# Performance work log

Hardware: AMD Instinct MI355X
Metric: run time of the kernel (lower is better)

The kernel has to match this reference:

```python
import jax, jax.numpy as jnp
import numpy as np

N = 50000
E = 800000
IN_DIM = 256
HID = 128
OUT = 64


def setup_inputs() -> dict:
    key = jax.random.key(0)
    ks = jax.random.split(key, 12)
    inp = {}
    inp["x"] = jax.random.normal(ks[0], (N, IN_DIM), dtype=jnp.float32)
    inp["edge_index"] = jax.random.randint(ks[1], (2, E), 0, N, dtype=jnp.int64)
    s0 = 1.0 / np.sqrt(IN_DIM)
    inp["W0"] = jax.random.uniform(ks[2], (IN_DIM, HID), jnp.float32, -s0, s0)
    inp["b0"] = jax.random.uniform(ks[3], (HID,), jnp.float32, -s0, s0)
    sa = 1.0 / np.sqrt(2 * HID)
    inp["att_w1"] = jax.random.uniform(ks[4], (2 * HID, 1), jnp.float32, -sa, sa)
    inp["att_b1"] = jax.random.uniform(ks[5], (1,), jnp.float32, -sa, sa)
    inp["eps1"] = jnp.float32(0.1)
    inp["att_w2"] = jax.random.uniform(ks[6], (2 * HID, 1), jnp.float32, -sa, sa)
    inp["att_b2"] = jax.random.uniform(ks[7], (1,), jnp.float32, -sa, sa)
    inp["eps2"] = jnp.float32(0.1)
    sc = 1.0 / np.sqrt(HID)
    inp["Wc"] = jax.random.uniform(ks[8], (HID, OUT), jnp.float32, -sc, sc)
    inp["bc"] = jax.random.uniform(ks[9], (OUT,), jnp.float32, -sc, sc)
    return inp


def _fagcn_layer(x, row, col, att_w, att_b, eps):
    # x: [N, H]; row/col: [E]
    x_i = x[row]                       # [E, H] source (gathered)
    x_j = x[col]                       # [E, H] destination
    # cat([x_i, x_j]) @ att_w == x_i @ att_w[:H] + x_j @ att_w[H:]
    H = x.shape[1]
    score = x_i @ att_w[:H] + x_j @ att_w[H:] + att_b  # [E, 1]
    alpha = jnp.tanh(score)            # [E, 1]
    messages = alpha * x_i             # [E, H]
    agg = jax.ops.segment_sum(messages, col, num_segments=x.shape[0])  # [N, H]
    return eps * x + (1.0 - eps) * agg


def reference(x, edge_index, W0, b0, att_w1, att_b1, eps1, att_w2, att_b2, eps2, Wc, bc):
    row, col = edge_index[0], edge_index[1]
    h = jax.nn.relu(x @ W0 + b0)       # initial linear + relu (dropout=eval identity)
    h = jax.nn.relu(_fagcn_layer(h, row, col, att_w1, att_b1, eps1))
    h = jax.nn.relu(_fagcn_layer(h, row, col, att_w2, att_b2, eps2))
    return h @ Wc + bc                 # [N, OUT]
```

## Files before the change

### kernel.cpp

```cpp
#include <hip/hip_runtime.h>

#define N_NODES 50000
#define E_EDGES 800000
#define IN_DIM 256
#define HID 128
#define OUT_DIM 64
#define SLOT 64

#define LR 64
#define KS 64
#define KP 72
#define HP 136

#define NBUILD ((E_EDGES / 8 + 255) / 256)
#define NLIN ((N_NODES + LR - 1) / LR)

typedef unsigned short u16;
typedef __attribute__((ext_vector_type(8))) short short8;
typedef __attribute__((ext_vector_type(4))) float floatx4;

__device__ __forceinline__ u16 f2bf(float f) {
    unsigned u = __float_as_uint(f);
    unsigned r = (u + 0x7FFFu + ((u >> 16) & 1u)) >> 16;
    return (u16)r;
}
__device__ __forceinline__ void bf8_unpack(uint4 v, float* f) {
    f[0] = __uint_as_float(v.x << 16); f[1] = __uint_as_float(v.x & 0xffff0000u);
    f[2] = __uint_as_float(v.y << 16); f[3] = __uint_as_float(v.y & 0xffff0000u);
    f[4] = __uint_as_float(v.z << 16); f[5] = __uint_as_float(v.z & 0xffff0000u);
    f[6] = __uint_as_float(v.w << 16); f[7] = __uint_as_float(v.w & 0xffff0000u);
}
__device__ __forceinline__ uint4 bf8_pack(const float* f) {
    uint4 o;
    o.x = f2bf(f[0]) | ((unsigned)f2bf(f[1]) << 16);
    o.y = f2bf(f[2]) | ((unsigned)f2bf(f[3]) << 16);
    o.z = f2bf(f[4]) | ((unsigned)f2bf(f[5]) << 16);
    o.w = f2bf(f[6]) | ((unsigned)f2bf(f[7]) << 16);
    return o;
}

__global__ __launch_bounds__(256) void k_front(
    const float* __restrict__ x, const float* __restrict__ W0,
    const float* __restrict__ b0, const float* __restrict__ aw1,
    u16* __restrict__ h, float* __restrict__ sa, float* __restrict__ sb,
    const int* __restrict__ ei, int* __restrict__ cnt,
    u16* __restrict__ srcidx, const float* __restrict__ Wc,
    u16* __restrict__ Wct) {
    __shared__ u16 As[LR][KP];
    __shared__ u16 Bs[HID][KP];

    if (blockIdx.x < NBUILD) {
        const int gid = blockIdx.x * 256 + threadIdx.x;
        if (gid < HID * OUT_DIM)
            Wct[gid] = f2bf(Wc[(gid & 127) * OUT_DIM + (gid >> 7)]);
        if (gid >= E_EDGES / 8) return;
        const int4 w0 = ((const int4*)ei)[2 * gid];
        const int4 w1 = ((const int4*)ei)[2 * gid + 1];
        const int4 c0 = ((const int4*)(ei + E_EDGES))[2 * gid];
        const int4 c1 = ((const int4*)(ei + E_EDGES))[2 * gid + 1];
        const int p0 = atomicAdd(&cnt[c0.x], 1);
        const int p1 = atomicAdd(&cnt[c0.y], 1);
        const int p2 = atomicAdd(&cnt[c0.z], 1);
        const int p3 = atomicAdd(&cnt[c0.w], 1);
        const int p4 = atomicAdd(&cnt[c1.x], 1);
        const int p5 = atomicAdd(&cnt[c1.y], 1);
        const int p6 = atomicAdd(&cnt[c1.z], 1);
        const int p7 = atomicAdd(&cnt[c1.w], 1);
        if (p0 < SLOT) srcidx[(c0.x << 6) + p0] = (u16)w0.x;
        if (p1 < SLOT) srcidx[(c0.y << 6) + p1] = (u16)w0.y;
        if (p2 < SLOT) srcidx[(c0.z << 6) + p2] = (u16)w0.z;
        if (p3 < SLOT) srcidx[(c0.w << 6) + p3] = (u16)w0.w;
        if (p4 < SLOT) srcidx[(c1.x << 6) + p4] = (u16)w1.x;
        if (p5 < SLOT) srcidx[(c1.y << 6) + p5] = (u16)w1.y;
        if (p6 < SLOT) srcidx[(c1.z << 6) + p6] = (u16)w1.z;
        if (p7 < SLOT) srcidx[(c1.w << 6) + p7] = (u16)w1.w;
        return;
    }

    const int t = threadIdx.x;
    const int lane = t & 63;
    const int w = t >> 6;
    const int sub = lane & 15;
    const int quad = lane >> 4;
    const int row0 = (blockIdx.x - NBUILD) * LR;

    floatx4 acc[8];
    #pragma unroll
    for (int i = 0; i < 8; ++i) acc[i] = (floatx4){0.f, 0.f, 0.f, 0.f};

    const int ar = t >> 2;
    const int ak = (t & 3) * 16;
    const int sr = t >> 1;
    const int sk = (t & 1) * 32;

    for (int k0 = 0; k0 < IN_DIM; k0 += KS) {
        {
            int gr = row0 + ar;
            if (gr > N_NODES - 1) gr = N_NODES - 1;
            const float* src = x + (size_t)gr * IN_DIM + k0 + ak;
            #pragma unroll
            for (int i = 0; i < 2; ++i) {
                float4 f0 = ((const float4*)src)[2 * i];
                float4 f1 = ((const float4*)src)[2 * i + 1];
                uint4 p;
                p.x = f2bf(f0.x) | ((unsigned)f2bf(f0.y) << 16);
                p.y = f2bf(f0.z) | ((unsigned)f2bf(f0.w) << 16);
                p.z = f2bf(f1.x) | ((unsigned)f2bf(f1.y) << 16);
                p.w = f2bf(f1.z) | ((unsigned)f2bf(f1.w) << 16);
                *(uint4*)&As[ar][ak + 8 * i] = p;
            }
            const float* wp = W0 + (size_t)(k0 + sk) * HID + sr;
            #pragma unroll
            for (int i = 0; i < 4; ++i) {
                uint4 p;
                unsigned q[4];
                #pragma unroll
                for (int j = 0; j < 4; ++j) {
                    const float lo = wp[(i * 8 + 2 * j) * HID];
                    const float hi = wp[(i * 8 + 2 * j + 1) * HID];
                    q[j] = f2bf(lo) | ((unsigned)f2bf(hi) << 16);
                }
                p.x = q[0]; p.y = q[1]; p.z = q[2]; p.w = q[3];
                *(uint4*)&Bs[sr][sk + 8 * i] = p;
            }
        }
        __syncthreads();
        #pragma unroll
        for (int kk = 0; kk < KS; kk += 32) {
            short8 a0 = *(const short8*)&As[w * 16 + sub][kk + quad * 8];
            #pragma unroll
            for (int ct = 0; ct < 8; ++ct) {
                short8 bb = *(const short8*)&Bs[ct * 16 + sub][kk + quad * 8];
                acc[ct] = __builtin_amdgcn_mfma_f32_16x16x32_bf16(a0, bb, acc[ct], 0, 0, 0);
            }
        }
        __syncthreads();
    }

    float bias[8], w1c[8], w2c[8];
    #pragma unroll
    for (int ct = 0; ct < 8; ++ct) {
        const int col = ct * 16 + sub;
        bias[ct] = b0[col];
        w1c[ct] = aw1[col];
        w2c[ct] = aw1[HID + col];
    }
    #pragma unroll
    for (int reg = 0; reg < 4; ++reg) {
        const int gr = row0 + w * 16 + quad * 4 + reg;
        const bool ok = gr < N_NODES;
        float ps = 0.f, pd = 0.f;
        #pragma unroll
        for (int ct = 0; ct < 8; ++ct) {
            const float val = fmaxf(acc[ct][reg] + bias[ct], 0.f);
            if (ok) h[(size_t)gr * HID + ct * 16 + sub] = f2bf(val);
            ps += val * w1c[ct];
            pd += val * w2c[ct];
        }
        #pragma unroll
        for (int off = 1; off < 16; off <<= 1) {
            ps += __shfl_xor(ps, off);
            pd += __shfl_xor(pd, off);
        }
        if (sub == 0 && ok) { sa[gr] = ps; sb[gr] = pd; }
    }
}

__global__ __launch_bounds__(256) void k_agg(const u16* __restrict__ hin,
                                             const float* __restrict__ sa,
                                             const float* __restrict__ sb,
                                             const float* __restrict__ attb,
                                             const float* __restrict__ epsp,
                                             const int* __restrict__ cnt,
                                             const u16* __restrict__ srcidx,
                                             u16* __restrict__ hout,
                                             const float* __restrict__ attw_next,
                                             float* __restrict__ sa_next,
                                             float* __restrict__ sb_next) {
    const int qid = threadIdx.x >> 4;
    const int sub = threadIdx.x & 15;
    const int n = blockIdx.x * 16 + qid;
    if (n >= N_NODES) return;
    const float b = attb[0];
    const float sbn = sb[n];
    const int beg = n << 6;
    int deg = cnt[n];
    if (deg > SLOT) deg = SLOT;
    const int end = beg + deg;
    float acc[8];
    #pragma unroll
    for (int j = 0; j < 8; ++j) acc[j] = 0.f;

    int e = beg;
    uint4 svn;
    if (e + 8 <= end) svn = *(const uint4*)(srcidx + e);
    for (; e + 8 <= end; e += 8) {
        const uint4 sv = svn;
        if (e + 16 <= end) svn = *(const uint4*)(srcidx + e + 8);
        int s[8];
        s[0] = (int)(sv.x & 0xffffu); s[1] = (int)(sv.x >> 16);
        s[2] = (int)(sv.y & 0xffffu); s[3] = (int)(sv.y >> 16);
        s[4] = (int)(sv.z & 0xffffu); s[5] = (int)(sv.z >> 16);
        s[6] = (int)(sv.w & 0xffffu); s[7] = (int)(sv.w >> 16);
        uint4 v[8];
        #pragma unroll
        for (int i = 0; i < 8; ++i)
            v[i] = *(const uint4*)(hin + (size_t)s[i] * HID + sub * 8);
        const float tt = tanhf(sa[s[sub & 7]] + sbn + b);
        float al[8];
        #pragma unroll
        for (int i = 0; i < 8; ++i) al[i] = __shfl(tt, i, 16);
        #pragma unroll
        for (int i = 0; i < 8; ++i) {
            float f[8];
            bf8_unpack(v[i], f);
            #pragma unroll
            for (int j = 0; j < 8; ++j) acc[j] += al[i] * f[j];
        }
    }
    const int rem = end - e;
    if (rem > 0) {
        const int sfirst = (int)srcidx[e];
        int s[8];
        #pragma unroll
        for (int i = 0; i < 8; ++i) s[i] = (i < rem) ? (int)srcidx[e + i] : sfirst;
        const float tt = ((sub & 7) < rem) ? tanhf(sa[s[sub & 7]] + sbn + b) : 0.f;
        float al[8];
        #pragma unroll
        for (int i = 0; i < 8; ++i) al[i] = __shfl(tt, i, 16);
        #pragma unroll
        for (int i = 0; i < 8; ++i) {
            if (i < rem) {
                const uint4 v = *(const uint4*)(hin + (size_t)s[i] * HID + sub * 8);
                float f[8];
                bf8_unpack(v, f);
                #pragma unroll
                for (int j = 0; j < 8; ++j) acc[j] += al[i] * f[j];
            }
        }
    }

    const float eps = epsp[0];
    const float om = 1.f - eps;
    const uint4 sv = *(const uint4*)(hin + (size_t)n * HID + sub * 8);
    float self[8], hv[8];
    bf8_unpack(sv, self);
    #pragma unroll
    for (int j = 0; j < 8; ++j)
        hv[j] = fmaxf(eps * self[j] + om * acc[j], 0.f);
    *(uint4*)(hout + (size_t)n * HID + sub * 8) = bf8_pack(hv);

    if (attw_next != nullptr) {
        float psum = 0.f, dsum = 0.f;
        #pragma unroll
        for (int j = 0; j < 8; ++j) {
            psum += hv[j] * attw_next[sub * 8 + j];
            dsum += hv[j] * attw_next[HID + sub * 8 + j];
        }
        #pragma unroll
        for (int off = 1; off < 16; off <<= 1) {
            psum += __shfl_xor(psum, off);
            dsum += __shfl_xor(dsum, off);
        }
        if (sub == 0) { sa_next[n] = psum; sb_next[n] = dsum; }
    }
}

__global__ __launch_bounds__(256) void k_out_mfma(const u16* __restrict__ h,
                                                  const u16* __restrict__ Wct,
                                                  const float* __restrict__ bc,
                                                  float* __restrict__ out) {
    __shared__ u16 Hs[LR][HP];
    const int t = threadIdx.x;
    const int lane = t & 63;
    const int w = t >> 6;
    const int sub = lane & 15;
    const int quad = lane >> 4;
    const int row0 = blockIdx.x * LR;

    {
        const int hr = t >> 2;
        const int hc = (t & 3) * 32;
        int gr = row0 + hr;
        if (gr > N_NODES - 1) gr = N_NODES - 1;
        const u16* src = h + (size_t)gr * HID + hc;
        #pragma unroll
        for (int i = 0; i < 4; ++i)
            *(uint4*)&Hs[hr][hc + 8 * i] = ((const uint4*)src)[i];
    }
    __syncthreads();

    floatx4 acc[4];
    #pragma unroll
    for (int j = 0; j < 4; ++j) acc[j] = (floatx4){0.f, 0.f, 0.f, 0.f};

    #pragma unroll
    for (int ks = 0; ks < 4; ++ks) {
        const int ko = ks * 32 + quad * 8;
        short8 a = *(const short8*)&Hs[w * 16 + sub][ko];
        #pragma unroll
        for (int ct = 0; ct < 4; ++ct) {
            short8 bb = *(const short8*)(Wct + (ct * 16 + sub) * HID + ko);
            acc[ct] = __builtin_amdgcn_mfma_f32_16x16x32_bf16(a, bb, acc[ct], 0, 0, 0);
        }
    }

    #pragma unroll
    for (int ct = 0; ct < 4; ++ct) {
        const float bias = bc[ct * 16 + sub];
        #pragma unroll
        for (int reg = 0; reg < 4; ++reg) {
            const int gr = row0 + w * 16 + quad * 4 + reg;
            if (gr < N_NODES)
                out[(size_t)gr * OUT_DIM + ct * 16 + sub] = acc[ct][reg] + bias;
        }
    }
}

extern "C" void kernel_launch(void* const* d_in, const int* in_sizes, int n_in,
                              void* d_out, int out_size, void* d_ws, size_t ws_size,
                              hipStream_t stream) {
    const float* x   = (const float*)d_in[0];
    const int*   ei  = (const int*)d_in[1];
    const float* W0  = (const float*)d_in[2];
    const float* b0  = (const float*)d_in[3];
    const float* aw1 = (const float*)d_in[4];
    const float* ab1 = (const float*)d_in[5];
    const float* e1  = (const float*)d_in[6];
    const float* aw2 = (const float*)d_in[7];
    const float* ab2 = (const float*)d_in[8];
    const float* e2  = (const float*)d_in[9];
    const float* Wc  = (const float*)d_in[10];
    const float* bc  = (const float*)d_in[11];
    float* out = (float*)d_out;

    u16* hA  = (u16*)d_ws;
    u16* hB  = hA + (size_t)N_NODES * HID;
    u16* Wct = hB + (size_t)N_NODES * HID;
    float* sa1 = (float*)(Wct + HID * OUT_DIM);
    float* sb1 = sa1 + N_NODES;
    float* sa2 = sb1 + N_NODES;
    float* sb2 = sa2 + N_NODES;
    int* cnt    = (int*)(sb2 + N_NODES);
    u16* srcidx = (u16*)(cnt + N_NODES);

    hipMemsetAsync(cnt, 0, N_NODES * sizeof(int), stream);
    k_front<<<NBUILD + NLIN, 256, 0, stream>>>(x, W0, b0, aw1, hA, sa1, sb1,
                                               ei, cnt, srcidx, Wc, Wct);
    k_agg<<<(N_NODES + 15) / 16, 256, 0, stream>>>(hA, sa1, sb1, ab1, e1, cnt, srcidx,
                                                   hB, aw2, sa2, sb2);
    k_agg<<<(N_NODES + 15) / 16, 256, 0, stream>>>(hB, sa2, sb2, ab2, e2, cnt, srcidx,
                                                   hA, nullptr, nullptr, nullptr);
    k_out_mfma<<<(N_NODES + LR - 1) / LR, 256, 0, stream>>>(hA, Wct, bc, out);
}
```

Baseline: 243.5 us.

## Fuse output linear layer into second aggregation kernel

Removes the separate MFMA output kernel and computes h@Wc+bc directly inside the second aggregation pass, using Wc staged in shared memory per block and lane shuffles to broadcast hidden values. This avoids writing and re-reading the final hidden tensor and one kernel launch, and drops the Wc transpose in the front kernel. In exchange every block reloads the full fp32 Wc into LDS (34KB), which may reduce occupancy of the latency-bound gather, and the projection now uses scalar FMAs instead of matrix cores.

```diff
diff --git a/kernel.cpp b/kernel.cpp
--- a/kernel.cpp
+++ b/kernel.cpp
@@ -10,7 +10,7 @@
 #define LR 64
 #define KS 64
 #define KP 72
-#define HP 136
+#define WCP 68
 
 #define NBUILD ((E_EDGES / 8 + 255) / 256)
 #define NLIN ((N_NODES + LR - 1) / LR)
@@ -44,15 +44,12 @@
     const float* __restrict__ b0, const float* __restrict__ aw1,
     u16* __restrict__ h, float* __restrict__ sa, float* __restrict__ sb,
     const int* __restrict__ ei, int* __restrict__ cnt,
-    u16* __restrict__ srcidx, const float* __restrict__ Wc,
-    u16* __restrict__ Wct) {
+    u16* __restrict__ srcidx) {
     __shared__ u16 As[LR][KP];
     __shared__ u16 Bs[HID][KP];
 
     if (blockIdx.x < NBUILD) {
         const int gid = blockIdx.x * 256 + threadIdx.x;
-        if (gid < HID * OUT_DIM)
-            Wct[gid] = f2bf(Wc[(gid & 127) * OUT_DIM + (gid >> 7)]);
         if (gid >= E_EDGES / 8) return;
         const int4 w0 = ((const int4*)ei)[2 * gid];
         const int4 w1 = ((const int4*)ei)[2 * gid + 1];
@@ -166,6 +163,7 @@
     }
 }
 
+template <bool FUSE_OUT>
 __global__ __launch_bounds__(256) void k_agg(const u16* __restrict__ hin,
                                              const float* __restrict__ sa,
                                              const float* __restrict__ sb,
@@ -176,7 +174,19 @@
                                              u16* __restrict__ hout,
                                              const float* __restrict__ attw_next,
                                              float* __restrict__ sa_next,
-                                             float* __restrict__ sb_next) {
+                                             float* __restrict__ sb_next,
+                                             const float* __restrict__ Wc,
+                                             const float* __restrict__ bc,
+                                             float* __restrict__ outp) {
+    __shared__ float Wcs[FUSE_OUT ? HID * WCP : 1];
+    if constexpr (FUSE_OUT) {
+        for (int i = threadIdx.x; i < HID * (OUT_DIM / 4); i += 256) {
+            const int k = i >> 4, c = (i & 15) << 2;
+            *(float4*)&Wcs[k * WCP + c] = *(const float4*)(Wc + k * OUT_DIM + c);
+        }
+        __syncthreads();
+    }
+
     const int qid = threadIdx.x >> 4;
     const int sub = threadIdx.x & 15;
     const int n = blockIdx.x * 16 + qid;
@@ -248,9 +258,9 @@
     #pragma unroll
     for (int j = 0; j < 8; ++j)
         hv[j] = fmaxf(eps * self[j] + om * acc[j], 0.f);
-    *(uint4*)(hout + (size_t)n * HID + sub * 8) = bf8_pack(hv);
-
-    if (attw_next != nullptr) {
+
+    if constexpr (!FUSE_OUT) {
+        *(uint4*)(hout + (size_t)n * HID + sub * 8) = bf8_pack(hv);
         float psum = 0.f, dsum = 0.f;
         #pragma unroll
         for (int j = 0; j < 8; ++j) {
@@ -263,57 +273,19 @@
             dsum += __shfl_xor(dsum, off);
         }
         if (sub == 0) { sa_next[n] = psum; sb_next[n] = dsum; }
-    }
-}
-
-__global__ __launch_bounds__(256) void k_out_mfma(const u16* __restrict__ h,
-                                                  const u16* __restrict__ Wct,
-                                                  const float* __restrict__ bc,
-                                                  float* __restrict__ out) {
-    __shared__ u16 Hs[LR][HP];
-    const int t = threadIdx.x;
-    const int lane = t & 63;
-    const int w = t >> 6;
-    const int sub = lane & 15;
-    const int quad = lane >> 4;
-    const int row0 = blockIdx.x * LR;
-
-    {
-        const int hr = t >> 2;
-        const int hc = (t & 3) * 32;
-        int gr = row0 + hr;
-        if (gr > N_NODES - 1) gr = N_NODES - 1;
-        const u16* src = h + (size_t)gr * HID + hc;
-        #pragma unroll
-        for (int i = 0; i < 4; ++i)
-            *(uint4*)&Hs[hr][hc + 8 * i] = ((const uint4*)src)[i];
-    }
-    __syncthreads();
-
-    floatx4 acc[4];
-    #pragma unroll
-    for (int j = 0; j < 4; ++j) acc[j] = (floatx4){0.f, 0.f, 0.f, 0.f};
-
-    #pragma unroll
-    for (int ks = 0; ks < 4; ++ks) {
-        const int ko = ks * 32 + quad * 8;
-        short8 a = *(const short8*)&Hs[w * 16 + sub][ko];
-        #pragma unroll
-        for (int ct = 0; ct < 4; ++ct) {
-            short8 bb = *(const short8*)(Wct + (ct * 16 + sub) * HID + ko);
-            acc[ct] = __builtin_amdgcn_mfma_f32_16x16x32_bf16(a, bb, acc[ct], 0, 0, 0);
-        }
-    }
-
-    #pragma unroll
-    for (int ct = 0; ct < 4; ++ct) {
-        const float bias = bc[ct * 16 + sub];
-        #pragma unroll
-        for (int reg = 0; reg < 4; ++reg) {
-            const int gr = row0 + w * 16 + quad * 4 + reg;
-            if (gr < N_NODES)
-                out[(size_t)gr * OUT_DIM + ct * 16 + sub] = acc[ct][reg] + bias;
-        }
+    } else {
+        float p0 = 0.f, p1 = 0.f, p2 = 0.f, p3 = 0.f;
+        #pragma unroll
+        for (int k = 0; k < HID; ++k) {
+            const float hvk = __shfl(hv[k & 7], k >> 3, 16);
+            const float4 wc = *(const float4*)&Wcs[k * WCP + sub * 4];
+            p0 += hvk * wc.x; p1 += hvk * wc.y;
+            p2 += hvk * wc.z; p3 += hvk * wc.w;
+        }
+        const float4 bb = *(const float4*)(bc + sub * 4);
+        float4 o4;
+        o4.x = p0 + bb.x; o4.y = p1 + bb.y; o4.z = p2 + bb.z; o4.w = p3 + bb.w;
+        *(float4*)(outp + (size_t)n * OUT_DIM + sub * 4) = o4;
     }
 }
 
@@ -336,8 +308,7 @@
 
     u16* hA  = (u16*)d_ws;
     u16* hB  = hA + (size_t)N_NODES * HID;
-    u16* Wct = hB + (size_t)N_NODES * HID;
-    float* sa1 = (float*)(Wct + HID * OUT_DIM);
+    float* sa1 = (float*)(hB + (size_t)N_NODES * HID);
     float* sb1 = sa1 + N_NODES;
     float* sa2 = sb1 + N_NODES;
     float* sb2 = sa2 + N_NODES;
@@ -346,10 +317,11 @@
 
     hipMemsetAsync(cnt, 0, N_NODES * sizeof(int), stream);
     k_front<<<NBUILD + NLIN, 256, 0, stream>>>(x, W0, b0, aw1, hA, sa1, sb1,
-                                               ei, cnt, srcidx, Wc, Wct);
-    k_agg<<<(N_NODES + 15) / 16, 256, 0, stream>>>(hA, sa1, sb1, ab1, e1, cnt, srcidx,
-                                                   hB, aw2, sa2, sb2);
-    k_agg<<<(N_NODES + 15) / 16, 256, 0, stream>>>(hB, sa2, sb2, ab2, e2, cnt, srcidx,
-                                                   hA, nullptr, nullptr, nullptr);
-    k_out_mfma<<<(N_NODES + LR - 1) / LR, 256, 0, stream>>>(hA, Wct, bc, out);
-}
+                                               ei, cnt, srcidx);
+    k_agg<false><<<(N_NODES + 15) / 16, 256, 0, stream>>>(
+        hA, sa1, sb1, ab1, e1, cnt, srcidx, hB, aw2, sa2, sb2,
+        nullptr, nullptr, nullptr);
+    k_agg<true><<<(N_NODES + 15) / 16, 256, 0, stream>>>(
+        hB, sa2, sb2, ab2, e2, cnt, srcidx, nullptr, nullptr, nullptr, nullptr,
+        Wc, bc, out);
+}
```

New measurement: 249.4 us. 2.4% more time.

## Pre-transpose weights to bf16 and feed MFMA operands directly from global memory

Applied to the files above, without the earlier changes.

Adds a small prep kernel that zeroes the degree counters in place of the memset and converts W0 and Wc into transposed bf16 layouts. The front linear layer and the output layer then drop their shared-memory staging and barriers, loading A fragments straight from x or h and B fragments from the transposed weights held in L2/L1. This removes the per-block strided fp32 W0 reads and conversions, the LDS traffic and the syncthreads, at the cost of one more launch and redundant per-wave global loads of the weight tiles.

```diff
diff --git a/kernel.cpp b/kernel.cpp
--- a/kernel.cpp
+++ b/kernel.cpp
@@ -8,10 +8,6 @@
 #define SLOT 64
 
 #define LR 64
-#define KS 64
-#define KP 72
-#define HP 136
-
 #define NBUILD ((E_EDGES / 8 + 255) / 256)
 #define NLIN ((N_NODES + LR - 1) / LR)
 
@@ -39,20 +35,31 @@
     return o;
 }
 
+__global__ __launch_bounds__(256) void k_pre(const float* __restrict__ W0,
+                                             const float* __restrict__ Wc,
+                                             u16* __restrict__ W0T,
+                                             u16* __restrict__ Wct,
+                                             int* __restrict__ cnt) {
+    const int gid = blockIdx.x * 256 + threadIdx.x;
+    if (gid < N_NODES / 4) ((int4*)cnt)[gid] = (int4){0, 0, 0, 0};
+    if (gid < IN_DIM * HID) {
+        const int n = gid >> 8, k = gid & (IN_DIM - 1);
+        W0T[gid] = f2bf(W0[k * HID + n]);
+    }
+    if (gid < HID * OUT_DIM) {
+        const int o = gid >> 7, k = gid & (HID - 1);
+        Wct[gid] = f2bf(Wc[k * OUT_DIM + o]);
+    }
+}
+
 __global__ __launch_bounds__(256) void k_front(
-    const float* __restrict__ x, const float* __restrict__ W0,
+    const float* __restrict__ x, const u16* __restrict__ W0T,
     const float* __restrict__ b0, const float* __restrict__ aw1,
     u16* __restrict__ h, float* __restrict__ sa, float* __restrict__ sb,
     const int* __restrict__ ei, int* __restrict__ cnt,
-    u16* __restrict__ srcidx, const float* __restrict__ Wc,
-    u16* __restrict__ Wct) {
-    __shared__ u16 As[LR][KP];
-    __shared__ u16 Bs[HID][KP];
-
+    u16* __restrict__ srcidx) {
     if (blockIdx.x < NBUILD) {
         const int gid = blockIdx.x * 256 + threadIdx.x;
-        if (gid < HID * OUT_DIM)
-            Wct[gid] = f2bf(Wc[(gid & 127) * OUT_DIM + (gid >> 7)]);
         if (gid >= E_EDGES / 8) return;
         const int4 w0 = ((const int4*)ei)[2 * gid];
         const int4 w1 = ((const int4*)ei)[2 * gid + 1];
@@ -84,57 +91,29 @@
     const int quad = lane >> 4;
     const int row0 = (blockIdx.x - NBUILD) * LR;
 
+    int gr_a = row0 + w * 16 + sub;
+    if (gr_a > N_NODES - 1) gr_a = N_NODES - 1;
+    const float* xrow = x + (size_t)gr_a * IN_DIM + quad * 8;
+    const u16* wbase = W0T + (size_t)sub * IN_DIM + quad * 8;
+
     floatx4 acc[8];
     #pragma unroll
     for (int i = 0; i < 8; ++i) acc[i] = (floatx4){0.f, 0.f, 0.f, 0.f};
 
-    const int ar = t >> 2;
-    const int ak = (t & 3) * 16;
-    const int sr = t >> 1;
-    const int sk = (t & 1) * 32;
-
-    for (int k0 = 0; k0 < IN_DIM; k0 += KS) {
-        {
-            int gr = row0 + ar;
-            if (gr > N_NODES - 1) gr = N_NODES - 1;
-            const float* src = x + (size_t)gr * IN_DIM + k0 + ak;
-            #pragma unroll
-            for (int i = 0; i < 2; ++i) {
-                float4 f0 = ((const float4*)src)[2 * i];
-                float4 f1 = ((const float4*)src)[2 * i + 1];
-                uint4 p;
-                p.x = f2bf(f0.x) | ((unsigned)f2bf(f0.y) << 16);
-                p.y = f2bf(f0.z) | ((unsigned)f2bf(f0.w) << 16);
-                p.z = f2bf(f1.x) | ((unsigned)f2bf(f1.y) << 16);
-                p.w = f2bf(f1.z) | ((unsigned)f2bf(f1.w) << 16);
-                *(uint4*)&As[ar][ak + 8 * i] = p;
-            }
-            const float* wp = W0 + (size_t)(k0 + sk) * HID + sr;
-            #pragma unroll
-            for (int i = 0; i < 4; ++i) {
-                uint4 p;
-                unsigned q[4];
-                #pragma unroll
-                for (int j = 0; j < 4; ++j) {
-                    const float lo = wp[(i * 8 + 2 * j) * HID];
-                    const float hi = wp[(i * 8 + 2 * j + 1) * HID];
-                    q[j] = f2bf(lo) | ((unsigned)f2bf(hi) << 16);
-                }
-                p.x = q[0]; p.y = q[1]; p.z = q[2]; p.w = q[3];
-                *(uint4*)&Bs[sr][sk + 8 * i] = p;
-            }
-        }
-        __syncthreads();
-        #pragma unroll
-        for (int kk = 0; kk < KS; kk += 32) {
-            short8 a0 = *(const short8*)&As[w * 16 + sub][kk + quad * 8];
-            #pragma unroll
-            for (int ct = 0; ct < 8; ++ct) {
-                short8 bb = *(const short8*)&Bs[ct * 16 + sub][kk + quad * 8];
-                acc[ct] = __builtin_amdgcn_mfma_f32_16x16x32_bf16(a0, bb, acc[ct], 0, 0, 0);
-            }
-        }
-        __syncthreads();
+    #pragma unroll
+    for (int ks = 0; ks < IN_DIM; ks += 32) {
+        const float4 f0 = *(const float4*)(xrow + ks);
+        const float4 f1 = *(const float4*)(xrow + ks + 4);
+        union { uint4 u; short8 s; } a;
+        a.u.x = f2bf(f0.x) | ((unsigned)f2bf(f0.y) << 16);
+        a.u.y = f2bf(f0.z) | ((unsigned)f2bf(f0.w) << 16);
+        a.u.z = f2bf(f1.x) | ((unsigned)f2bf(f1.y) << 16);
+        a.u.w = f2bf(f1.z) | ((unsigned)f2bf(f1.w) << 16);
+        #pragma unroll
+        for (int ct = 0; ct < 8; ++ct) {
+            const short8 bb = *(const short8*)(wbase + ct * 16 * IN_DIM + ks);
+            acc[ct] = __builtin_amdgcn_mfma_f32_16x16x32_bf16(a.s, bb, acc[ct], 0, 0, 0);
+        }
     }
 
     float bias[8], w1c[8], w2c[8];
@@ -270,7 +249,6 @@
                                                   const u16* __restrict__ Wct,
                                                   const float* __restrict__ bc,
                                                   float* __restrict__ out) {
-    __shared__ u16 Hs[LR][HP];
     const int t = threadIdx.x;
     const int lane = t & 63;
     const int w = t >> 6;
@@ -278,29 +256,21 @@
     const int quad = lane >> 4;
     const int row0 = blockIdx.x * LR;
 
-    {
-        const int hr = t >> 2;
-        const int hc = (t & 3) * 32;
-        int gr = row0 + hr;
-        if (gr > N_NODES - 1) gr = N_NODES - 1;
-        const u16* src = h + (size_t)gr * HID + hc;
-        #pragma unroll
-        for (int i = 0; i < 4; ++i)
-            *(uint4*)&Hs[hr][hc + 8 * i] = ((const uint4*)src)[i];
-    }
-    __syncthreads();
+    int gr_a = row0 + w * 16 + sub;
+    if (gr_a > N_NODES - 1) gr_a = N_NODES - 1;
+    const u16* hrow = h + (size_t)gr_a * HID + quad * 8;
+    const u16* wbase = Wct + (size_t)sub * HID + quad * 8;
 
     floatx4 acc[4];
     #pragma unroll
     for (int j = 0; j < 4; ++j) acc[j] = (floatx4){0.f, 0.f, 0.f, 0.f};
 
     #pragma unroll
-    for (int ks = 0; ks < 4; ++ks) {
-        const int ko = ks * 32 + quad * 8;
-        short8 a = *(const short8*)&Hs[w * 16 + sub][ko];
+    for (int ks = 0; ks < HID; ks += 32) {
+        const short8 a = *(const short8*)(hrow + ks);
         #pragma unroll
         for (int ct = 0; ct < 4; ++ct) {
-            short8 bb = *(const short8*)(Wct + (ct * 16 + sub) * HID + ko);
+            const short8 bb = *(const short8*)(wbase + ct * 16 * HID + ks);
             acc[ct] = __builtin_amdgcn_mfma_f32_16x16x32_bf16(a, bb, acc[ct], 0, 0, 0);
         }
     }
@@ -336,7 +306,8 @@
 
     u16* hA  = (u16*)d_ws;
     u16* hB  = hA + (size_t)N_NODES * HID;
-    u16* Wct = hB + (size_t)N_NODES * HID;
+    u16* W0T = hB + (size_t)N_NODES * HID;
+    u16* Wct = W0T + IN_DIM * HID;
     float* sa1 = (float*)(Wct + HID * OUT_DIM);
     float* sb1 = sa1 + N_NODES;
     float* sa2 = sb1 + N_NODES;
@@ -344,12 +315,12 @@
     int* cnt    = (int*)(sb2 + N_NODES);
     u16* srcidx = (u16*)(cnt + N_NODES);
 
-    hipMemsetAsync(cnt, 0, N_NODES * sizeof(int), stream);
-    k_front<<<NBUILD + NLIN, 256, 0, stream>>>(x, W0, b0, aw1, hA, sa1, sb1,
-                                               ei, cnt, srcidx, Wc, Wct);
+    k_pre<<<128, 256, 0, stream>>>(W0, Wc, W0T, Wct, cnt);
+    k_front<<<NBUILD + NLIN, 256, 0, stream>>>(x, W0T, b0, aw1, hA, sa1, sb1,
+                                               ei, cnt, srcidx);
     k_agg<<<(N_NODES + 15) / 16, 256, 0, stream>>>(hA, sa1, sb1, ab1, e1, cnt, srcidx,
                                                    hB, aw2, sa2, sb2);
     k_agg<<<(N_NODES + 15) / 16, 256, 0, stream>>>(hB, sa2, sb2, ab2, e2, cnt, srcidx,
                                                    hA, nullptr, nullptr, nullptr);
-    k_out_mfma<<<(N_NODES + LR - 1) / LR, 256, 0, stream>>>(hA, Wct, bc, out);
-}
+    k_out_mfma<<<NLIN, 256, 0, stream>>>(hA, Wct, bc, out);
+}
```

New measurement: 255.4 us. 1.05x slower.
